# Kernel optimization log

Hardware: AMD Instinct MI355X
Metric: run time of the kernel (lower is better)

The kernel has to match this reference:

```python
import jax, jax.numpy as jnp
import numpy as np
from math import sqrt


def setup_inputs() -> dict:
    key = jax.random.key(0)
    ks = jax.random.split(key, 10)
    N, C = 192, 96  # C = N // 2
    n, h, w = 8, 64, 64
    s = lambda fan_in: 1.0 / np.sqrt(fan_in)
    return {
        "x": jax.random.normal(ks[0], (n, N, h, w), dtype=jnp.float32),
        "pe": jax.random.normal(ks[1], (N, 120, 120), dtype=jnp.float32) * 0.02,
        "wq": jax.random.normal(ks[2], (C, N), dtype=jnp.float32) * s(N),
        "bq": jax.random.normal(ks[3], (C,), dtype=jnp.float32) * 0.01,
        "wk": jax.random.normal(ks[4], (C, N), dtype=jnp.float32) * s(N),
        "bk": jax.random.normal(ks[5], (C,), dtype=jnp.float32) * 0.01,
        "wv": jax.random.normal(ks[6], (C, N), dtype=jnp.float32) * s(N),
        "bv": jax.random.normal(ks[7], (C,), dtype=jnp.float32) * 0.01,
        "wz": jax.random.normal(ks[8], (N, C), dtype=jnp.float32) * s(C),
        "bz": jax.random.normal(ks[9], (N,), dtype=jnp.float32) * 0.01,
    }


def _conv1x1(x, w, b):
    # x: [n, cin, h, w]; w: [cout, cin]; b: [cout]
    return jnp.einsum("oc,nchw->nohw", w, x) + b[None, :, None, None]


def reference(x, pe, wq, bq, wk, bk, wv, bv, wz, bz):
    n, c_in, h, w = x.shape
    hw = h * w
    # 2D positional encoding, sliced to the actual spatial size
    x = x + pe[None, :, :h, :w]
    c = wq.shape[0]  # N // 2
    q = _conv1x1(x, wq, bq).reshape(n, c, hw)   # [n, c, hw]
    k = _conv1x1(x, wk, bk).reshape(n, c, hw)   # [n, c, hw]
    v = _conv1x1(x, wv, bv).reshape(n, c, hw)   # [n, c, hw]
    scale = sqrt(hw)
    # logits[n, i, j] = sum_c q[n,c,i] * k[n,c,j]
    logits = jnp.einsum("nci,ncj->nij", q, k) / scale  # [n, hw, hw]
    weights = jax.nn.softmax(logits, axis=-1)
    # z[n, c, i] = sum_j weights[n,i,j] * v[n,c,j]
    z = jnp.einsum("nij,ncj->nci", weights, v).reshape(n, c, h, w)
    z = _conv1x1(z, wz, bz)  # [n, N, h, w]
    return x + z
```

## Files before the change

### kernel.cpp

```cpp
#include <hip/hip_runtime.h>
#include <hip/hip_bf16.h>

#define HW 4096
#define CIN 192
#define CMID 96

typedef __attribute__((ext_vector_type(8))) short bf16x8;
typedef __attribute__((ext_vector_type(4))) float f32x4;
typedef __attribute__((ext_vector_type(16))) float f32x16;
typedef __attribute__((ext_vector_type(4))) unsigned int u32x4;

static __device__ __forceinline__ unsigned short f2bf(float f) {
    union { float f; unsigned int u; } v;
    v.f = f;
    unsigned int r = v.u + 0x7fffu + ((v.u >> 16) & 1u);
    return (unsigned short)(r >> 16);
}

#define SCQ (0.015625f * 1.44269504089f)

__global__ __launch_bounds__(256) void convw_kernel(
    const float* __restrict__ wq, const float* __restrict__ wk,
    const float* __restrict__ wv, const float* __restrict__ wz,
    unsigned short* __restrict__ wqkvb, unsigned short* __restrict__ wzb)
{
    int idx = blockIdx.x * 256 + threadIdx.x;
    if (idx < 3 * CMID * CIN) {
        int m = idx / (CMID * CIN), r = idx % (CMID * CIN);
        const float* w = (m == 0) ? wq : ((m == 1) ? wk : wv);
        wqkvb[idx] = f2bf(w[r]);
    } else if (idx < 3 * CMID * CIN + CIN * CMID) {
        int r = idx - 3 * CMID * CIN;
        wzb[r] = f2bf(wz[r]);
    }
}

__global__ __launch_bounds__(512) void qkv_kernel(
    const float* __restrict__ x, const float* __restrict__ pe,
    const unsigned short* __restrict__ wqkvb,
    const float* __restrict__ bq, const float* __restrict__ bk,
    const float* __restrict__ bv,
    unsigned short* __restrict__ QF, unsigned short* __restrict__ KF,
    unsigned short* __restrict__ VF)
{
    const int n = blockIdx.y, bx = blockIdx.x, i0 = bx * 64, t = threadIdx.x;
    __shared__ unsigned short xt[64 * 200];

    #pragma unroll
    for (int it = 0; it < 6; ++it) {
        int q = t + it * 512;
        int c = q >> 4, il4 = (q & 15) << 2;
        f32x4 xv = *(const f32x4*)(x + ((size_t)n * CIN + c) * HW + i0 + il4);
        f32x4 pv = *(const f32x4*)(pe + c * 14400 + bx * 120 + il4);
        float a0 = xv[0] + pv[0], a1 = xv[1] + pv[1];
        float a2 = xv[2] + pv[2], a3 = xv[3] + pv[3];
        unsigned w01, w23;
        asm("v_cvt_pk_bf16_f32 %0, %1, %2" : "=v"(w01) : "v"(a0), "v"(a1));
        asm("v_cvt_pk_bf16_f32 %0, %1, %2" : "=v"(w23) : "v"(a2), "v"(a3));
        xt[(il4 + 0) * 200 + c] = (unsigned short)w01;
        xt[(il4 + 1) * 200 + c] = (unsigned short)(w01 >> 16);
        xt[(il4 + 2) * 200 + c] = (unsigned short)w23;
        xt[(il4 + 3) * 200 + c] = (unsigned short)(w23 >> 16);
    }
    __syncthreads();

    const int w = t >> 6, lane = t & 63, l15 = lane & 15, lg = lane >> 4;
    const int wg = w >> 2;
    const int p0 = (w & 3) * 16;

    bf16x8 af[6];
    #pragma unroll
    for (int f = 0; f < 6; ++f)
        af[f] = *(const bf16x8*)(xt + (p0 + l15) * 200 + f * 32 + lg * 8);

    #pragma unroll
    for (int cc = 0; cc < 9; ++cc) {
        const int ct = wg * 9 + cc;
        const int m = ct / 6, c6 = ct % 6;
        f32x4 acc = (f32x4){0.f, 0.f, 0.f, 0.f};
        const unsigned short* wrow = wqkvb + (ct * 16 + l15) * CIN + lg * 8;
        #pragma unroll
        for (int f = 0; f < 6; ++f) {
            bf16x8 wf = *(const bf16x8*)(wrow + f * 32);
            if (m < 2)
                acc = __builtin_amdgcn_mfma_f32_16x16x32_bf16(wf, af[f], acc, 0, 0, 0);
            else
                acc = __builtin_amdgcn_mfma_f32_16x16x32_bf16(af[f], wf, acc, 0, 0, 0);
        }
        if (m < 2) {
            f32x4 bv4 = *(const f32x4*)(((m == 0) ? bq : bk) + c6 * 16 + lg * 4);
            ushort4 pk4;
            if (m == 0) {
                pk4.x = f2bf((acc[0] + bv4[0]) * SCQ);
                pk4.y = f2bf((acc[1] + bv4[1]) * SCQ);
                pk4.z = f2bf((acc[2] + bv4[2]) * SCQ);
                pk4.w = f2bf((acc[3] + bv4[3]) * SCQ);
            } else {
                pk4.x = f2bf(acc[0] + bv4[0]);
                pk4.y = f2bf(acc[1] + bv4[1]);
                pk4.z = f2bf(acc[2] + bv4[2]);
                pk4.w = f2bf(acc[3] + bv4[3]);
            }
            const int p = i0 + p0 + l15;
            unsigned short* dst = (m == 0) ? QF : KF;
            size_t fa = ((((size_t)n * 128 + (p >> 5)) * 6 + c6) * 64
                         + (lg >> 1) * 32 + (p & 31)) * 8 + (lg & 1) * 4;
            *(ushort4*)(dst + fa) = pk4;
        } else {
            const float bias = bv[c6 * 16 + l15];
            ushort4 pk4;
            pk4.x = f2bf(acc[0] + bias); pk4.y = f2bf(acc[1] + bias);
            pk4.z = f2bf(acc[2] + bias); pk4.w = f2bf(acc[3] + bias);
            const int ch = c6 * 16 + l15;
            const int slot = 2 * (w & 3) + (lg >> 1);
            size_t fa = ((((((size_t)n * 64 + bx) * 3 + (ch >> 5)) * 2
                           + (slot >> 2)) * 2 + ((slot >> 1) & 1)) * 64
                         + (slot & 1) * 32 + (ch & 31)) * 8 + (lg & 1) * 4;
            *(ushort4*)(VF + fa) = pk4;
        }
    }
}

__global__ __launch_bounds__(256, 2) void attn_kernel(
    const unsigned short* __restrict__ QF, const unsigned short* __restrict__ KF,
    const unsigned short* __restrict__ VF,
    unsigned short* __restrict__ zp, float* __restrict__ lp)
{
    const int bid = blockIdx.x;
    const int n    = bid & 7;
    const int iblk = (bid >> 3) & 15;
    const int js   = bid >> 7;

    const int t = threadIdx.x, w = t >> 6, lane = t & 63;
    const int l31 = lane & 31, hi = lane >> 5;
    const int ib = iblk * 256 + w * 64;

    const unsigned short* QFb = QF + (size_t)n * 128 * 3072;
    const unsigned short* KFb = KF + (size_t)n * 128 * 3072;
    const unsigned short* VFb = VF + (size_t)n * 64 * 6144;

    bf16x8 qf[2][6];
    #pragma unroll
    for (int is = 0; is < 2; ++is)
        #pragma unroll
        for (int kc = 0; kc < 6; ++kc)
            qf[is][kc] = *(const bf16x8*)(QFb + ((size_t)((ib >> 5) + is) * 6 + kc) * 512
                                          + lane * 8);

    f32x16 O[2][3];
    #pragma unroll
    for (int is = 0; is < 2; ++is)
        #pragma unroll
        for (int cc = 0; cc < 3; ++cc)
            #pragma unroll
            for (int e = 0; e < 16; ++e) O[is][cc][e] = 0.f;
    float lsum0 = 0.f, lsum1 = 0.f;

    for (int tt = 0; tt < 32; ++tt) {
        const int jt = js * 32 + tt;
        const unsigned short* Kt = KFb + (size_t)jt * 3072;

        bf16x8 kf[6];
        #pragma unroll
        for (int kc = 0; kc < 6; ++kc)
            kf[kc] = *(const bf16x8*)(Kt + kc * 512 + lane * 8);
        bf16x8 vf[2][3];
        #pragma unroll
        for (int jc = 0; jc < 2; ++jc)
            #pragma unroll
            for (int cc = 0; cc < 3; ++cc)
                vf[jc][cc] = *(const bf16x8*)(VFb
                    + ((size_t)((jt >> 1) * 3 + cc) * 4 + (jt & 1) * 2 + jc) * 512
                    + lane * 8);

        f32x16 s0, s1;
        #pragma unroll
        for (int e = 0; e < 16; ++e) { s0[e] = 0.f; s1[e] = 0.f; }
        __builtin_amdgcn_s_setprio(1);
        #pragma unroll
        for (int kc = 0; kc < 6; ++kc) {
            s0 = __builtin_amdgcn_mfma_f32_32x32x16_bf16(kf[kc], qf[0][kc], s0, 0, 0, 0);
            s1 = __builtin_amdgcn_mfma_f32_32x32x16_bf16(kf[kc], qf[1][kc], s1, 0, 0, 0);
        }
        __builtin_amdgcn_s_setprio(0);

        unsigned pkk[2][4][2];
        #pragma unroll
        for (int q = 0; q < 4; ++q)
            #pragma unroll
            for (int rp = 0; rp < 2; ++rp) {
                float lo0 = __builtin_exp2f(s0[q * 4 + 2 * rp]);
                float hh0 = __builtin_exp2f(s0[q * 4 + 2 * rp + 1]);
                float lo1 = __builtin_exp2f(s1[q * 4 + 2 * rp]);
                float hh1 = __builtin_exp2f(s1[q * 4 + 2 * rp + 1]);
                lsum0 += lo0 + hh0;
                lsum1 += lo1 + hh1;
                asm("v_cvt_pk_bf16_f32 %0, %1, %2"
                    : "=v"(pkk[0][q][rp]) : "v"(lo0), "v"(hh0));
                asm("v_cvt_pk_bf16_f32 %0, %1, %2"
                    : "=v"(pkk[1][q][rp]) : "v"(lo1), "v"(hh1));
            }

        u32x4 pfu[2][2];
        #pragma unroll
        for (int is = 0; is < 2; ++is)
            #pragma unroll
            for (int jc = 0; jc < 2; ++jc) {
                unsigned x0 = pkk[is][2 * jc][0], y0 = pkk[is][2 * jc + 1][0];
                unsigned x1 = pkk[is][2 * jc][1], y1 = pkk[is][2 * jc + 1][1];
                asm("v_permlane32_swap_b32 %0, %1" : "+v"(y0), "+v"(x0));
                asm("v_permlane32_swap_b32 %0, %1" : "+v"(y1), "+v"(x1));
                pfu[is][jc][0] = x0; pfu[is][jc][1] = x1;
                pfu[is][jc][2] = y0; pfu[is][jc][3] = y1;
            }

        __builtin_amdgcn_s_setprio(1);
        #pragma unroll
        for (int jc = 0; jc < 2; ++jc) {
            bf16x8 pa0 = __builtin_bit_cast(bf16x8, pfu[0][jc]);
            bf16x8 pa1 = __builtin_bit_cast(bf16x8, pfu[1][jc]);
            #pragma unroll
            for (int cc = 0; cc < 3; ++cc) {
                O[0][cc] = __builtin_amdgcn_mfma_f32_32x32x16_bf16(pa0, vf[jc][cc], O[0][cc], 0, 0, 0);
                O[1][cc] = __builtin_amdgcn_mfma_f32_32x32x16_bf16(pa1, vf[jc][cc], O[1][cc], 0, 0, 0);
            }
        }
        __builtin_amdgcn_s_setprio(0);
    }

    unsigned short* zb = zp + ((size_t)js * 8 + n) * HW * CMID;
    #pragma unroll
    for (int is = 0; is < 2; ++is)
        #pragma unroll
        for (int cc = 0; cc < 3; ++cc)
            #pragma unroll
            for (int r = 0; r < 16; ++r) {
                int i = ib + is * 32 + (r & 3) + 8 * (r >> 2) + 4 * hi;
                zb[(size_t)i * CMID + cc * 32 + l31] = f2bf(O[is][cc][r]);
            }

    lsum0 += __shfl_xor(lsum0, 32, 64);
    lsum1 += __shfl_xor(lsum1, 32, 64);
    if (hi == 0) {
        float* lb = lp + ((size_t)js * 8 + n) * HW;
        lb[ib + l31]      = lsum0;
        lb[ib + 32 + l31] = lsum1;
    }
}

__global__ __launch_bounds__(256) void zproj_kernel(
    const unsigned short* __restrict__ zp, const float* __restrict__ lp,
    const unsigned short* __restrict__ wzb, const float* __restrict__ bz,
    const float* __restrict__ x, const float* __restrict__ pe,
    float* __restrict__ out)
{
    const int n = blockIdx.y, i0 = blockIdx.x * 64, t = threadIdx.x;
    __shared__ unsigned short zt[64 * 104];
    __shared__ float ll[64];

    if (t < 64) {
        float s = 0.f;
        #pragma unroll
        for (int sl = 0; sl < 4; ++sl)
            s += lp[(size_t)sl * 8 * HW + (size_t)n * HW + i0 + t];
        ll[t] = 1.f / s;
    }
    __syncthreads();

    #pragma unroll
    for (int u = 0; u < 3; ++u) {
        int unit = t + u * 256;
        int i = unit / 12, g = unit % 12;
        size_t gidx = ((size_t)n * HW + i0 + i) * CMID + g * 8;
        float a[8];
        #pragma unroll
        for (int e = 0; e < 8; ++e) a[e] = 0.f;
        #pragma unroll
        for (int sl = 0; sl < 4; ++sl) {
            u32x4 wv = *(const u32x4*)(zp + (size_t)sl * 8 * HW * CMID + gidx);
            #pragma unroll
            for (int k = 0; k < 4; ++k) {
                union { unsigned u; float f; } lo, hi2;
                lo.u = wv[k] << 16;
                hi2.u = wv[k] & 0xffff0000u;
                a[2 * k]     += lo.f;
                a[2 * k + 1] += hi2.f;
            }
        }
        float li = ll[i];
        unsigned ww[4];
        #pragma unroll
        for (int k = 0; k < 4; ++k) {
            float p0 = a[2 * k] * li, p1 = a[2 * k + 1] * li;
            asm("v_cvt_pk_bf16_f32 %0, %1, %2" : "=v"(ww[k]) : "v"(p0), "v"(p1));
        }
        u32x4 wv4 = {ww[0], ww[1], ww[2], ww[3]};
        *(u32x4*)(zt + i * 104 + g * 8) = wv4;
    }
    __syncthreads();

    const int w = t >> 6, lane = t & 63, l15 = lane & 15, lg = lane >> 4;
    const int p0 = w * 16;

    bf16x8 af[3];
    #pragma unroll
    for (int f = 0; f < 3; ++f)
        af[f] = *(const bf16x8*)(zt + (p0 + l15) * 104 + f * 32 + lg * 8);

    #pragma unroll
    for (int ct = 0; ct < 12; ++ct) {
        f32x4 acc = (f32x4){0.f, 0.f, 0.f, 0.f};
        const unsigned short* wrow = wzb + (ct * 16 + l15) * CMID + lg * 8;
        #pragma unroll
        for (int f = 0; f < 3; ++f) {
            bf16x8 wf = *(const bf16x8*)(wrow + f * 32);
            acc = __builtin_amdgcn_mfma_f32_16x16x32_bf16(af[f], wf, acc, 0, 0, 0);
        }
        const int co = ct * 16 + l15;
        const int ibase = i0 + p0 + lg * 4;
        size_t xa = ((size_t)n * CIN + co) * HW + ibase;
        f32x4 xv = *(const f32x4*)(x + xa);
        f32x4 pv = *(const f32x4*)(pe + co * 14400 + blockIdx.x * 120 + p0 + lg * 4);
        const float bias = bz[co];
        f32x4 o;
        #pragma unroll
        for (int r = 0; r < 4; ++r) o[r] = xv[r] + pv[r] + acc[r] + bias;
        *(f32x4*)(out + xa) = o;
    }
}

extern "C" void kernel_launch(void* const* d_in, const int* in_sizes, int n_in,
                              void* d_out, int out_size, void* d_ws, size_t ws_size,
                              hipStream_t stream) {
    const float* x  = (const float*)d_in[0];
    const float* pe = (const float*)d_in[1];
    const float* wq = (const float*)d_in[2];
    const float* bq = (const float*)d_in[3];
    const float* wk = (const float*)d_in[4];
    const float* bk = (const float*)d_in[5];
    const float* wv = (const float*)d_in[6];
    const float* bv = (const float*)d_in[7];
    const float* wz = (const float*)d_in[8];
    const float* bz = (const float*)d_in[9];
    float* out = (float*)d_out;

    char* ws = (char*)d_ws;
    unsigned short* wqkvb = (unsigned short*)(ws);
    unsigned short* wzb   = (unsigned short*)(ws + 131072);
    unsigned short* QFb   = (unsigned short*)(ws + 196608);
    unsigned short* KFb   = (unsigned short*)(ws + 6488064);
    unsigned short* VFb   = (unsigned short*)(ws + 12779520);
    unsigned short* zpb   = (unsigned short*)(ws + 19070976);
    float*          lpb   = (float*)(ws + 44236800);

    convw_kernel<<<288, 256, 0, stream>>>(wq, wk, wv, wz, wqkvb, wzb);
    qkv_kernel<<<dim3(64, 8), 512, 0, stream>>>(x, pe, wqkvb, bq, bk, bv,
                                                QFb, KFb, VFb);
    attn_kernel<<<512, 256, 0, stream>>>(QFb, KFb, VFb, zpb, lpb);
    zproj_kernel<<<dim3(64, 8), 256, 0, stream>>>(zpb, lpb, wzb, bz, x, pe, out);
}
```

Before: 118.0 us.

## Halve per-wave query tile in attention kernel and double grid size

Each attention wave now processes one 32-row query subtile instead of two, and the grid doubles to 1024 blocks to cover the same work. This cuts accumulator and fragment registers per thread, allowing more waves in flight and more blocks to spread across CUs. In exchange, each K and V fragment loaded from memory feeds half as many MFMAs, doubling K/V load traffic per unit of compute.

```diff
diff --git a/kernel.cpp b/kernel.cpp
--- a/kernel.cpp
+++ b/kernel.cpp
@@ -128,33 +128,29 @@
 {
     const int bid = blockIdx.x;
     const int n    = bid & 7;
-    const int iblk = (bid >> 3) & 15;
-    const int js   = bid >> 7;
+    const int iblk = (bid >> 3) & 31;
+    const int js   = bid >> 8;
 
     const int t = threadIdx.x, w = t >> 6, lane = t & 63;
     const int l31 = lane & 31, hi = lane >> 5;
-    const int ib = iblk * 256 + w * 64;
+    const int ib = iblk * 128 + w * 32;
 
     const unsigned short* QFb = QF + (size_t)n * 128 * 3072;
     const unsigned short* KFb = KF + (size_t)n * 128 * 3072;
     const unsigned short* VFb = VF + (size_t)n * 64 * 6144;
 
-    bf16x8 qf[2][6];
-    #pragma unroll
-    for (int is = 0; is < 2; ++is)
-        #pragma unroll
-        for (int kc = 0; kc < 6; ++kc)
-            qf[is][kc] = *(const bf16x8*)(QFb + ((size_t)((ib >> 5) + is) * 6 + kc) * 512
-                                          + lane * 8);
-
-    f32x16 O[2][3];
-    #pragma unroll
-    for (int is = 0; is < 2; ++is)
-        #pragma unroll
-        for (int cc = 0; cc < 3; ++cc)
-            #pragma unroll
-            for (int e = 0; e < 16; ++e) O[is][cc][e] = 0.f;
-    float lsum0 = 0.f, lsum1 = 0.f;
+    bf16x8 qf[6];
+    #pragma unroll
+    for (int kc = 0; kc < 6; ++kc)
+        qf[kc] = *(const bf16x8*)(QFb + ((size_t)(ib >> 5) * 6 + kc) * 512
+                                  + lane * 8);
+
+    f32x16 O[3];
+    #pragma unroll
+    for (int cc = 0; cc < 3; ++cc)
+        #pragma unroll
+        for (int e = 0; e < 16; ++e) O[cc][e] = 0.f;
+    float lsum = 0.f;
 
     for (int tt = 0; tt < 32; ++tt) {
         const int jt = js * 32 + tt;
@@ -173,78 +169,62 @@
                     + ((size_t)((jt >> 1) * 3 + cc) * 4 + (jt & 1) * 2 + jc) * 512
                     + lane * 8);
 
-        f32x16 s0, s1;
-        #pragma unroll
-        for (int e = 0; e < 16; ++e) { s0[e] = 0.f; s1[e] = 0.f; }
+        f32x16 s0;
+        #pragma unroll
+        for (int e = 0; e < 16; ++e) s0[e] = 0.f;
         __builtin_amdgcn_s_setprio(1);
         #pragma unroll
-        for (int kc = 0; kc < 6; ++kc) {
-            s0 = __builtin_amdgcn_mfma_f32_32x32x16_bf16(kf[kc], qf[0][kc], s0, 0, 0, 0);
-            s1 = __builtin_amdgcn_mfma_f32_32x32x16_bf16(kf[kc], qf[1][kc], s1, 0, 0, 0);
-        }
+        for (int kc = 0; kc < 6; ++kc)
+            s0 = __builtin_amdgcn_mfma_f32_32x32x16_bf16(kf[kc], qf[kc], s0, 0, 0, 0);
         __builtin_amdgcn_s_setprio(0);
 
-        unsigned pkk[2][4][2];
+        unsigned pkk[4][2];
         #pragma unroll
         for (int q = 0; q < 4; ++q)
             #pragma unroll
             for (int rp = 0; rp < 2; ++rp) {
-                float lo0 = __builtin_exp2f(s0[q * 4 + 2 * rp]);
-                float hh0 = __builtin_exp2f(s0[q * 4 + 2 * rp + 1]);
-                float lo1 = __builtin_exp2f(s1[q * 4 + 2 * rp]);
-                float hh1 = __builtin_exp2f(s1[q * 4 + 2 * rp + 1]);
-                lsum0 += lo0 + hh0;
-                lsum1 += lo1 + hh1;
+                float lo = __builtin_exp2f(s0[q * 4 + 2 * rp]);
+                float hh = __builtin_exp2f(s0[q * 4 + 2 * rp + 1]);
+                lsum += lo + hh;
                 asm("v_cvt_pk_bf16_f32 %0, %1, %2"
-                    : "=v"(pkk[0][q][rp]) : "v"(lo0), "v"(hh0));
-                asm("v_cvt_pk_bf16_f32 %0, %1, %2"
-                    : "=v"(pkk[1][q][rp]) : "v"(lo1), "v"(hh1));
+                    : "=v"(pkk[q][rp]) : "v"(lo), "v"(hh));
             }
 
-        u32x4 pfu[2][2];
-        #pragma unroll
-        for (int is = 0; is < 2; ++is)
+        u32x4 pfu[2];
+        #pragma unroll
+        for (int jc = 0; jc < 2; ++jc) {
+            unsigned x0 = pkk[2 * jc][0], y0 = pkk[2 * jc + 1][0];
+            unsigned x1 = pkk[2 * jc][1], y1 = pkk[2 * jc + 1][1];
+            asm("v_permlane32_swap_b32 %0, %1" : "+v"(y0), "+v"(x0));
+            asm("v_permlane32_swap_b32 %0, %1" : "+v"(y1), "+v"(x1));
+            pfu[jc][0] = x0; pfu[jc][1] = x1;
+            pfu[jc][2] = y0; pfu[jc][3] = y1;
+        }
+
+        __builtin_amdgcn_s_setprio(1);
+        #pragma unroll
+        for (int jc = 0; jc < 2; ++jc) {
+            bf16x8 pa = __builtin_bit_cast(bf16x8, pfu[jc]);
             #pragma unroll
-            for (int jc = 0; jc < 2; ++jc) {
-                unsigned x0 = pkk[is][2 * jc][0], y0 = pkk[is][2 * jc + 1][0];
-                unsigned x1 = pkk[is][2 * jc][1], y1 = pkk[is][2 * jc + 1][1];
-                asm("v_permlane32_swap_b32 %0, %1" : "+v"(y0), "+v"(x0));
-                asm("v_permlane32_swap_b32 %0, %1" : "+v"(y1), "+v"(x1));
-                pfu[is][jc][0] = x0; pfu[is][jc][1] = x1;
-                pfu[is][jc][2] = y0; pfu[is][jc][3] = y1;
-            }
-
-        __builtin_amdgcn_s_setprio(1);
-        #pragma unroll
-        for (int jc = 0; jc < 2; ++jc) {
-            bf16x8 pa0 = __builtin_bit_cast(bf16x8, pfu[0][jc]);
-            bf16x8 pa1 = __builtin_bit_cast(bf16x8, pfu[1][jc]);
-            #pragma unroll
-            for (int cc = 0; cc < 3; ++cc) {
-                O[0][cc] = __builtin_amdgcn_mfma_f32_32x32x16_bf16(pa0, vf[jc][cc], O[0][cc], 0, 0, 0);
-                O[1][cc] = __builtin_amdgcn_mfma_f32_32x32x16_bf16(pa1, vf[jc][cc], O[1][cc], 0, 0, 0);
-            }
+            for (int cc = 0; cc < 3; ++cc)
+                O[cc] = __builtin_amdgcn_mfma_f32_32x32x16_bf16(pa, vf[jc][cc], O[cc], 0, 0, 0);
         }
         __builtin_amdgcn_s_setprio(0);
     }
 
     unsigned short* zb = zp + ((size_t)js * 8 + n) * HW * CMID;
     #pragma unroll
-    for (int is = 0; is < 2; ++is)
-        #pragma unroll
-        for (int cc = 0; cc < 3; ++cc)
-            #pragma unroll
-            for (int r = 0; r < 16; ++r) {
-                int i = ib + is * 32 + (r & 3) + 8 * (r >> 2) + 4 * hi;
-                zb[(size_t)i * CMID + cc * 32 + l31] = f2bf(O[is][cc][r]);
-            }
-
-    lsum0 += __shfl_xor(lsum0, 32, 64);
-    lsum1 += __shfl_xor(lsum1, 32, 64);
+    for (int cc = 0; cc < 3; ++cc)
+        #pragma unroll
+        for (int r = 0; r < 16; ++r) {
+            int i = ib + (r & 3) + 8 * (r >> 2) + 4 * hi;
+            zb[(size_t)i * CMID + cc * 32 + l31] = f2bf(O[cc][r]);
+        }
+
+    lsum += __shfl_xor(lsum, 32, 64);
     if (hi == 0) {
         float* lb = lp + ((size_t)js * 8 + n) * HW;
-        lb[ib + l31]      = lsum0;
-        lb[ib + 32 + l31] = lsum1;
+        lb[ib + l31] = lsum;
     }
 }
 
@@ -356,6 +336,6 @@
     convw_kernel<<<288, 256, 0, stream>>>(wq, wk, wv, wz, wqkvb, wzb);
     qkv_kernel<<<dim3(64, 8), 512, 0, stream>>>(x, pe, wqkvb, bq, bk, bv,
                                                 QFb, KFb, VFb);
-    attn_kernel<<<512, 256, 0, stream>>>(QFb, KFb, VFb, zpb, lpb);
+    attn_kernel<<<1024, 256, 0, stream>>>(QFb, KFb, VFb, zpb, lpb);
     zproj_kernel<<<dim3(64, 8), 256, 0, stream>>>(zpb, lpb, wzb, bz, x, pe, out);
 }
```

New measurement: 127.5 us. 8.0% more time.
